# Kernel optimization log

Hardware: AMD Instinct MI355X
Metric: run time of the kernel (lower is better)

## Reference

```python
import jax, jax.numpy as jnp
import numpy as np

N = 10000
E = 160000
IN_DIM = 512
OUT_DIM = 256
NEG_SLOPE = 0.2  # DGL GATConv default LeakyReLU slope


def _gat_conv(x, W, b, attn_l, attn_r, src, dst, num_nodes, heads, out_dim):
    """DGL GATConv (eval mode, feat_drop/attn_drop disabled).
    x: [N, F_in]; W: [F_in, heads*out]; b: [heads*out];
    attn_l/attn_r: [heads, out]. Returns [N, heads, out]."""
    h = (x @ W).reshape(num_nodes, heads, out_dim)            # [N,H,D]
    el = jnp.einsum('nhd,hd->nh', h, attn_l)                  # [N,H]
    er = jnp.einsum('nhd,hd->nh', h, attn_r)                  # [N,H]
    e = jax.nn.leaky_relu(el[src] + er[dst], NEG_SLOPE)       # [E,H]
    # destination-grouped (edge) softmax, numerically stable
    m = jax.ops.segment_max(e, dst, num_segments=num_nodes)   # [N,H], -inf for empty
    m = jnp.where(jnp.isfinite(m), m, 0.0)
    ee = jnp.exp(e - m[dst])                                  # [E,H]
    s = jax.ops.segment_sum(ee, dst, num_segments=num_nodes)  # [N,H]
    a = ee / jnp.where(s > 0, s, 1.0)[dst]                    # [E,H]
    # message aggregation: scatter-add a_e * h[src]
    out = jax.ops.segment_sum(a[:, :, None] * h[src], dst, num_segments=num_nodes)
    return out + b.reshape(1, heads, out_dim)


def setup_inputs() -> dict:
    key = jax.random.key(0)
    ks = jax.random.split(key, 16)
    def glorot(k, shape):
        fan = shape[0] + shape[-1] if len(shape) > 1 else shape[-1]
        return jax.random.normal(k, shape, dtype=jnp.float32) * np.sqrt(2.0 / fan)
    inp = {
        'x':   jax.random.normal(ks[0], (N, IN_DIM), dtype=jnp.float32),
        'src': jax.random.randint(ks[1], (E,), 0, N),
        'dst': jax.random.randint(ks[2], (E,), 0, N),
        'W1': glorot(ks[3], (IN_DIM, 10 * 128)),
        'b1': jnp.zeros((10 * 128,), jnp.float32),
        'al1': glorot(ks[4], (10, 128)),
        'ar1': glorot(ks[5], (10, 128)),
        'W2': glorot(ks[6], (1280, 10 * 64)),
        'b2': jnp.zeros((10 * 64,), jnp.float32),
        'al2': glorot(ks[7], (10, 64)),
        'ar2': glorot(ks[8], (10, 64)),
        'W3': glorot(ks[9], (640, OUT_DIM)),
        'b3': jnp.zeros((OUT_DIM,), jnp.float32),
        'al3': glorot(ks[10], (1, OUT_DIM)),
        'ar3': glorot(ks[11], (1, OUT_DIM)),
        # residual linear 512 -> 256
        'Wres': glorot(ks[12], (IN_DIM, OUT_DIM)),
        'bres': jnp.zeros((OUT_DIM,), jnp.float32),
        'fuse_weight': jnp.full((1,), 0.5, jnp.float32),
    }
    return inp


def reference(x, src, dst, W1, b1, al1, ar1, W2, b2, al2, ar2,
              W3, b3, al3, ar3, Wres, bres, fuse_weight):
    elu = jax.nn.elu
    res = elu(x @ Wres + bres)                                        # [N,256]
    s1 = elu(_gat_conv(x, W1, b1, al1, ar1, src, dst, N, 10, 128))
    s1 = s1.reshape(N, -1)                                            # [N,1280]
    s2 = elu(_gat_conv(s1, W2, b2, al2, ar2, src, dst, N, 10, 64))
    s2 = s2.reshape(N, -1)                                            # [N,640]
    s3 = elu(_gat_conv(s2, W3, b3, al3, ar3, src, dst, N, 1, OUT_DIM))
    s3 = s3.reshape(N, -1)                                            # [N,256]
    return fuse_weight * s3 + (1.0 - fuse_weight) * res
```

## Files before the change

### kernel.cpp

```cpp
#include <hip/hip_runtime.h>
#include <stdint.h>

#define DEVINL __device__ __forceinline__

typedef __attribute__((ext_vector_type(8))) short short8;
typedef __attribute__((ext_vector_type(4))) float f32x4;

static constexpr int NNODES = 10000;

DEVINL float bf2f(unsigned short u) {
  unsigned int x = ((unsigned int)u) << 16;
  float f;
  __builtin_memcpy(&f, &x, 4);
  return f;
}
DEVINL unsigned short f2bf(float f) {
  unsigned int x;
  __builtin_memcpy(&x, &f, 4);
  unsigned int lsb = (x >> 16) & 1;
  x += 0x7fffu + lsb;
  return (unsigned short)(x >> 16);
}
DEVINL void bfpair(unsigned int u, float& f0, float& f1) {
  unsigned int a = u << 16, b = u & 0xffff0000u;
  __builtin_memcpy(&f0, &a, 4);
  __builtin_memcpy(&f1, &b, 4);
}
DEVINL bool is_bf16_mode(const unsigned int* fwWord) {
  return ((*fwWord) & 0xFFFFu) == 0x3F00u;
}

DEVINL void async_cp16(void* lds, const void* g) {
  __builtin_amdgcn_global_load_lds((const __attribute__((address_space(1))) unsigned int*)g,
                                   (__attribute__((address_space(3))) unsigned int*)lds,
                                   16, 0, 0);
}

__global__ __launch_bounds__(256) void gemm_fused(const unsigned short* __restrict__ A,
                                                  const unsigned short* __restrict__ Bt,
                                                  unsigned short* __restrict__ Ch,
                                                  int M, int N, int K, int nres,
                                                  unsigned short* __restrict__ Cres,
                                                  const float* __restrict__ rbias,
                                                  float* __restrict__ elp,
                                                  float* __restrict__ erp,
                                                  const float* __restrict__ alf,
                                                  const float* __restrict__ arf,
                                                  int logD, int H) {
  __shared__ __align__(16) unsigned short lA[128 * 32];
  __shared__ __align__(16) unsigned short lB[128 * 32];
  const int tid = threadIdx.x;
  const int wid = tid >> 6;
  const int lane = tid & 63;
  const int tm = blockIdx.x * 128;
  const int tn = blockIdx.y * 128;
  const int wr = (wid >> 1) * 64;
  const int wc = (wid & 1) * 64;
  f32x4 acc[4][4] = {};
  const int r_in_chunk = lane >> 2;
  const int cb = (lane & 3) * 16;
  const int mr = lane & 15;
  const int kq = (lane >> 4) * 8;
  const size_t stride = (size_t)K * 2;

  for (int k0 = 0; k0 < K; k0 += 32) {
#pragma unroll
    for (int c = 0; c < 2; ++c) {
      const int chunk = wid * 2 + c;
      const int row = chunk * 16 + r_in_chunk;
      int ga = tm + row;
      if (ga >= M) ga = M - 1;
      async_cp16(&lA[chunk * 512], (const char*)A + (size_t)ga * stride + (size_t)k0 * 2 + cb);
      const int gb = tn + row;
      async_cp16(&lB[chunk * 512], (const char*)Bt + (size_t)gb * stride + (size_t)k0 * 2 + cb);
    }
    __syncthreads();
    short8 af[4], bf[4];
#pragma unroll
    for (int i = 0; i < 4; ++i)
      af[i] = *(const short8*)&lA[(wr + i * 16 + mr) * 32 + kq];
#pragma unroll
    for (int j = 0; j < 4; ++j)
      bf[j] = *(const short8*)&lB[(wc + j * 16 + mr) * 32 + kq];
#pragma unroll
    for (int i = 0; i < 4; ++i)
#pragma unroll
      for (int j = 0; j < 4; ++j)
        acc[i][j] = __builtin_amdgcn_mfma_f32_16x16x32_bf16(af[i], bf[j], acc[i][j], 0, 0, 0);
    __syncthreads();
  }

  const int rbase = (lane >> 4) * 4;
  const int cc = lane & 15;
  if (tn < nres) {
#pragma unroll
    for (int i = 0; i < 4; ++i)
#pragma unroll
      for (int r = 0; r < 4; ++r) {
        const int row = tm + wr + i * 16 + rbase + r;
        if (row < M) {
#pragma unroll
          for (int j = 0; j < 4; ++j) {
            const int col = tn + wc + j * 16 + cc;
            float v = acc[i][j][r] + rbias[col];
            v = v > 0.f ? v : (__expf(v) - 1.f);
            Cres[(size_t)row * nres + col] = f2bf(v);
          }
        }
      }
  } else {
    const int tnh = tn - nres;
    const int Nh = N - nres;
    const int colw = tnh + wc;
    const int head = colw >> logD;
#pragma unroll
    for (int i = 0; i < 4; ++i)
#pragma unroll
      for (int r = 0; r < 4; ++r) {
        const int row = tm + wr + i * 16 + rbase + r;
        if (row < M) {
#pragma unroll
          for (int j = 0; j < 4; ++j)
            Ch[(size_t)row * Nh + colw + j * 16 + cc] = f2bf(acc[i][j][r]);
        }
      }
    float alv[4], arv[4];
#pragma unroll
    for (int j = 0; j < 4; ++j) {
      alv[j] = alf[colw + j * 16 + cc];
      arv[j] = arf[colw + j * 16 + cc];
    }
#pragma unroll
    for (int i = 0; i < 4; ++i)
#pragma unroll
      for (int r = 0; r < 4; ++r) {
        float pe = 0.f, pr = 0.f;
#pragma unroll
        for (int j = 0; j < 4; ++j) {
          pe += acc[i][j][r] * alv[j];
          pr += acc[i][j][r] * arv[j];
        }
#pragma unroll
        for (int o = 1; o < 16; o <<= 1) {
          pe += __shfl_xor(pe, o);
          pr += __shfl_xor(pr, o);
        }
        const int row = tm + wr + i * 16 + rbase + r;
        if ((lane & 15) == 0 && row < M) {
          atomicAdd(&elp[(size_t)row * H + head], pe);
          atomicAdd(&erp[(size_t)row * H + head], pr);
        }
      }
  }
}

struct CvtJobs {
  const void* src[12];
  float* dst[12];
  int n[12];
  int cnt;
};
__global__ void cvt_small_f32(CvtJobs jobs, const unsigned int* fwWord) {
  const bool isb = is_bf16_mode(fwWord);
  for (int j = 0; j < jobs.cnt; ++j) {
    for (int i = blockIdx.x * blockDim.x + threadIdx.x; i < jobs.n[j];
         i += gridDim.x * blockDim.x) {
      jobs.dst[j][i] = isb ? bf2f(((const unsigned short*)jobs.src[j])[i])
                           : ((const float*)jobs.src[j])[i];
    }
  }
}

__global__ __launch_bounds__(256) void cvt_x_bf16(const void* __restrict__ in,
                                                  unsigned short* __restrict__ out,
                                                  long n, const unsigned int* fwWord) {
  const bool isb = is_bf16_mode(fwWord);
  const long i0 = (long)(blockIdx.x * 256 + threadIdx.x) * 8;
  if (i0 >= n) return;
  if (isb) {
    *(short8*)&out[i0] = *(const short8*)&((const unsigned short*)in)[i0];
  } else {
    const float* f = (const float*)in + i0;
    unsigned short r[8];
#pragma unroll
    for (int j = 0; j < 8; ++j) r[j] = f2bf(f[j]);
    *(short8*)&out[i0] = *(const short8*)r;
  }
}

struct TAll {
  const void* src[4];
  unsigned short* dst[4];
  int K[4];
  int N[4];
  int b0[5];
};
__global__ __launch_bounds__(256) void transp_all4(TAll ja, const unsigned int* fwWord) {
  const bool isb = is_bf16_mode(fwWord);
  __shared__ unsigned short t[32][33];
  const int bid = blockIdx.x;
  int j = 0;
  while (j < 3 && bid >= ja.b0[j + 1]) ++j;
  const int local = bid - ja.b0[j];
  const int K = ja.K[j], Nn = ja.N[j];
  const int tilesX = Nn / 32;
  const int bx = (local % tilesX) * 32;
  const int by = (local / tilesX) * 32;
  const void* W = ja.src[j];
  unsigned short* Wt = ja.dst[j];
  const int x = threadIdx.x;
  const int y0 = threadIdx.y;
  for (int y = y0; y < 32; y += 8) {
    const size_t idx = (size_t)(by + y) * Nn + bx + x;
    t[y][x] = isb ? ((const unsigned short*)W)[idx] : f2bf(((const float*)W)[idx]);
  }
  __syncthreads();
  for (int y = y0; y < 32; y += 8)
    Wt[(size_t)(bx + y) * K + by + x] = t[x][y];
}

template <int H>
__global__ __launch_bounds__(256) void edge_w(const float* __restrict__ el,
                                              const float* __restrict__ er,
                                              const int* __restrict__ sidx,
                                              const int* __restrict__ didx,
                                              float* __restrict__ we_t, int E) {
  const int p = blockIdx.x * 256 + threadIdx.x;
  if (p >= E) return;
  const float* ep = el + (size_t)sidx[p] * H;
  const float* rp = er + (size_t)didx[p] * H;
#pragma unroll
  for (int h = 0; h < H; ++h) {
    float sc = ep[h] + rp[h];
    sc = sc > 0.f ? sc : 0.2f * sc;
    we_t[(size_t)h * E + p] = __expf(sc);
  }
}

template <int H, int D, int NS, int CW, int MODE>
__global__ __launch_bounds__(64) void gat_agg_hs(const unsigned short* __restrict__ hf,
                                                 const float* __restrict__ we_t,
                                                 const int* __restrict__ sidx,
                                                 const int* __restrict__ rowstart,
                                                 const float* __restrict__ bias,
                                                 void* __restrict__ outp,
                                                 const unsigned short* __restrict__ resact,
                                                 const float* __restrict__ fwf,
                                                 const unsigned int* fwWord, int E) {
  constexpr int CHUNK = 64;
  constexpr int SF = H * D / NS;
  constexpr int ACT = SF / CW;
  constexpr int SROW = H * D * 2;
  constexpr int LOG2D = (D == 64) ? 6 : (D == 128) ? 7 : 8;
  static_assert((H * D) % NS == 0 && (SF % CW) == 0 && ACT <= 64, "geometry");
  static_assert(CW == 2 || CW == 4, "vector width");
  static_assert(SF < 2 * D, "slice spans at most 2 heads");
  __shared__ float wls[2 * (CHUNK + 1)];
  __shared__ int soff[CHUNK];

  const int bid = blockIdx.x;
  const int n = bid / NS;
  const int sl = bid % NS;
  const int tid = threadIdx.x;
  const int e0 = rowstart[n], e1 = rowstart[n + 1];
  const int f0 = SF * sl;
  const int hlo = f0 >> LOG2D;
  const int hhi = (f0 + SF - 1) >> LOG2D;
  const int fbase = f0 + tid * CW;
  const int wbase = ((fbase >> LOG2D) != hlo) ? (CHUNK + 1) : 0;
  const bool act = tid < ACT;
  const char* hfb = (const char*)(hf + fbase);
  float acc[CW] = {};
  float swlo = 0.f, swhi = 0.f;

  for (int cs = e0; cs < e1; cs += CHUNK) {
    const int ce = min(CHUNK, e1 - cs);
    if (tid < ce) {
      soff[tid] = sidx[cs + tid] * SROW;
      const float wlo = we_t[(size_t)hlo * E + cs + tid];
      wls[tid] = wlo;
      swlo += wlo;
      if (hhi != hlo) {
        const float whi = we_t[(size_t)hhi * E + cs + tid];
        wls[CHUNK + 1 + tid] = whi;
        swhi += whi;
      }
    }
    __syncthreads();
    if (act) {
      int j = 0;
      for (; j + 8 <= ce; j += 8) {
        int o[8];
        float w[8];
#pragma unroll
        for (int b = 0; b < 8; ++b) {
          o[b] = soff[j + b];
          w[b] = wls[wbase + j + b];
        }
        if constexpr (CW == 4) {
          uint2 u[8];
#pragma unroll
          for (int b = 0; b < 8; ++b) u[b] = *(const uint2*)(hfb + o[b]);
#pragma unroll
          for (int b = 0; b < 8; ++b) {
            float a0, a1, a2, a3;
            bfpair(u[b].x, a0, a1);
            bfpair(u[b].y, a2, a3);
            acc[0] += w[b] * a0; acc[1] += w[b] * a1;
            acc[2] += w[b] * a2; acc[3] += w[b] * a3;
          }
        } else {
          unsigned int u[8];
#pragma unroll
          for (int b = 0; b < 8; ++b) u[b] = *(const unsigned int*)(hfb + o[b]);
#pragma unroll
          for (int b = 0; b < 8; ++b) {
            float a0, a1;
            bfpair(u[b], a0, a1);
            acc[0] += w[b] * a0; acc[1] += w[b] * a1;
          }
        }
      }
      for (; j < ce; ++j) {
        const int o = soff[j];
        const float w = wls[wbase + j];
        if constexpr (CW == 4) {
          const uint2 u = *(const uint2*)(hfb + o);
          float a0, a1, a2, a3;
          bfpair(u.x, a0, a1);
          bfpair(u.y, a2, a3);
          acc[0] += w * a0; acc[1] += w * a1; acc[2] += w * a2; acc[3] += w * a3;
        } else {
          const unsigned int u = *(const unsigned int*)(hfb + o);
          float a0, a1;
          bfpair(u, a0, a1);
          acc[0] += w * a0; acc[1] += w * a1;
        }
      }
    }
    __syncthreads();
  }

#pragma unroll
  for (int o = 32; o; o >>= 1) {
    swlo += __shfl_xor(swlo, o);
    swhi += __shfl_xor(swhi, o);
  }
  if (!act) return;
  const float stot = wbase ? swhi : swlo;
  const float inv = stot > 0.f ? 1.f / stot : 0.f;
  const size_t obase = (size_t)n * (H * D) + fbase;
  float v[CW];
#pragma unroll
  for (int k = 0; k < CW; ++k) {
    v[k] = acc[k] * inv + bias[fbase + k];
    v[k] = v[k] > 0.f ? v[k] : (__expf(v[k]) - 1.f);
  }
  if (MODE == 0) {
#pragma unroll
    for (int k = 0; k < CW; ++k)
      ((unsigned short*)outp)[obase + k] = f2bf(v[k]);
  } else {
    const float fw = fwf[0];
    const bool outb = is_bf16_mode(fwWord);
#pragma unroll
    for (int k = 0; k < CW; ++k) {
      const float r = bf2f(resact[obase + k]);
      const float o = fw * v[k] + (1.f - fw) * r;
      if (outb) ((unsigned short*)outp)[obase + k] = f2bf(o);
      else      ((float*)outp)[obase + k] = o;
    }
  }
}

__global__ void sentinel_k(unsigned short* __restrict__ outp, int total) {
  const int i = blockIdx.x * 256 + threadIdx.x;
  if (i < total) outp[i] = f2bf(12344.0f);
}

__global__ void hist_k(const int* __restrict__ dst, int* __restrict__ deg, int E) {
  const int i = blockIdx.x * blockDim.x + threadIdx.x;
  if (i < E) atomicAdd(&deg[dst[i]], 1);
}

__global__ __launch_bounds__(1024) void scan_k(const int* __restrict__ deg,
                                               int* __restrict__ rowstart,
                                               int* __restrict__ cursor, int Nn) {
  __shared__ int ls[1024];
  const int tid = threadIdx.x;
  const int CH = (Nn + 1023) >> 10;
  const int start = tid * CH;
  int sum = 0;
  for (int i = 0; i < CH; ++i) {
    const int idx = start + i;
    if (idx < Nn) sum += deg[idx];
  }
  ls[tid] = sum;
  __syncthreads();
  for (int o = 1; o < 1024; o <<= 1) {
    int v = 0;
    if (tid >= o) v = ls[tid - o];
    __syncthreads();
    ls[tid] += v;
    __syncthreads();
  }
  int run = tid > 0 ? ls[tid - 1] : 0;
  for (int i = 0; i < CH; ++i) {
    const int idx = start + i;
    if (idx < Nn) {
      rowstart[idx] = run;
      cursor[idx] = run;
      run += deg[idx];
    }
  }
  if (tid == 1023) rowstart[Nn] = ls[1023];
}

__global__ void scatter_k(const int* __restrict__ dst, const int* __restrict__ srcA,
                          int* __restrict__ cursor, int* __restrict__ sidx,
                          int* __restrict__ didx, int E) {
  const int i = blockIdx.x * blockDim.x + threadIdx.x;
  if (i < E) {
    const int d = dst[i];
    const int p = atomicAdd(&cursor[d], 1);
    sidx[p] = srcA[i];
    didx[p] = d;
  }
}

extern "C" void kernel_launch(void* const* d_in, const int* in_sizes, int n_in,
                              void* d_out, int out_size, void* d_ws, size_t ws_size,
                              hipStream_t stream) {
  const void* x    = d_in[0];
  const int* src   = (const int*)d_in[1];
  const int* dstA  = (const int*)d_in[2];
  const void* W1   = d_in[3];
  const void* b1   = d_in[4];
  const void* al1  = d_in[5];
  const void* ar1  = d_in[6];
  const void* W2   = d_in[7];
  const void* b2   = d_in[8];
  const void* al2  = d_in[9];
  const void* ar2  = d_in[10];
  const void* W3   = d_in[11];
  const void* b3   = d_in[12];
  const void* al3  = d_in[13];
  const void* ar3  = d_in[14];
  const void* Wres = d_in[15];
  const void* bres = d_in[16];
  const void* fw   = d_in[17];
  const unsigned int* fwWord = (const unsigned int*)fw;
  const int E = in_sizes[1];
  const int M = NNODES;

  char* base = (char*)d_ws;
  size_t off = 0;
  auto alloc = [&](size_t bytes) -> char* {
    char* p = base + off;
    off = (off + bytes + 255) & ~(size_t)255;
    return p;
  };
  char* zbase   = base;
  int* deg      = (int*)alloc((size_t)M * 4);
  float* elb1   = (float*)alloc((size_t)M * 10 * 4);
  float* erb1   = (float*)alloc((size_t)M * 10 * 4);
  float* elb2   = (float*)alloc((size_t)M * 10 * 4);
  float* erb2   = (float*)alloc((size_t)M * 10 * 4);
  float* elb3   = (float*)alloc((size_t)M * 4);
  float* erb3   = (float*)alloc((size_t)M * 4);
  const size_t zbytes = off;
  int* rowstart = (int*)alloc((size_t)(M + 1) * 4);
  int* cursor   = (int*)alloc((size_t)M * 4);
  int* sidx     = (int*)alloc((size_t)E * 4);
  int* didx     = (int*)alloc((size_t)E * 4);
  float* we_t   = (float*)alloc((size_t)E * 10 * 4);
  float* b1f   = (float*)alloc(1280 * 4);
  float* al1f  = (float*)alloc(1280 * 4);
  float* ar1f  = (float*)alloc(1280 * 4);
  float* b2f   = (float*)alloc(640 * 4);
  float* al2f  = (float*)alloc(640 * 4);
  float* ar2f  = (float*)alloc(640 * 4);
  float* b3f   = (float*)alloc(256 * 4);
  float* al3f  = (float*)alloc(256 * 4);
  float* ar3f  = (float*)alloc(256 * 4);
  float* bresf = (float*)alloc(256 * 4);
  float* fwf   = (float*)alloc(4);
  unsigned short* wtcat  = (unsigned short*)alloc((size_t)1536 * 512 * 2);
  unsigned short* wt2    = (unsigned short*)alloc((size_t)640 * 1280 * 2);
  unsigned short* wt3    = (unsigned short*)alloc((size_t)256 * 640 * 2);
  unsigned short* resact = (unsigned short*)alloc((size_t)M * 256 * 2);
  unsigned short* regA   = (unsigned short*)alloc((size_t)M * 1280 * 2);
  unsigned short* regB   = (unsigned short*)alloc((size_t)M * 1280 * 2);

  if (off > ws_size) {
    sentinel_k<<<(out_size + 255) / 256, 256, 0, stream>>>((unsigned short*)d_out, out_size);
    return;
  }

  unsigned short* h1 = regA;
  unsigned short* h2 = regA;
  unsigned short* h3 = regA;
  unsigned short* xb = regB;
  unsigned short* s1 = regB;
  unsigned short* s2 = regB;

  hipMemsetAsync(zbase, 0, zbytes, stream);

  CvtJobs jobs;
  const void* srcs[11] = {b1, al1, ar1, b2, al2, ar2, b3, al3, ar3, bres, fw};
  float* dsts[11] = {b1f, al1f, ar1f, b2f, al2f, ar2f, b3f, al3f, ar3f, bresf, fwf};
  const int ns[11] = {1280, 1280, 1280, 640, 640, 640, 256, 256, 256, 256, 1};
  for (int j = 0; j < 11; ++j) { jobs.src[j] = srcs[j]; jobs.dst[j] = dsts[j]; jobs.n[j] = ns[j]; }
  jobs.cnt = 11;
  cvt_small_f32<<<8, 256, 0, stream>>>(jobs, fwWord);

  cvt_x_bf16<<<(int)(((long)M * 512 / 8 + 255) / 256), 256, 0, stream>>>(x, xb, (long)M * 512, fwWord);

  TAll ta;
  ta.src[0] = W1;   ta.dst[0] = wtcat + (size_t)256 * 512; ta.K[0] = 512;  ta.N[0] = 1280;
  ta.src[1] = W2;   ta.dst[1] = wt2;                       ta.K[1] = 1280; ta.N[1] = 640;
  ta.src[2] = W3;   ta.dst[2] = wt3;                       ta.K[2] = 640;  ta.N[2] = 256;
  ta.src[3] = Wres; ta.dst[3] = wtcat;                     ta.K[3] = 512;  ta.N[3] = 256;
  ta.b0[0] = 0;
  for (int j = 0; j < 4; ++j)
    ta.b0[j + 1] = ta.b0[j] + (ta.K[j] / 32) * (ta.N[j] / 32);
  transp_all4<<<ta.b0[4], dim3(32, 8), 0, stream>>>(ta, fwWord);

  hist_k<<<(E + 255) / 256, 256, 0, stream>>>(dstA, deg, E);
  scan_k<<<1, 1024, 0, stream>>>(deg, rowstart, cursor, M);
  scatter_k<<<(E + 255) / 256, 256, 0, stream>>>(dstA, src, cursor, sidx, didx, E);

  const int MT = (M + 127) / 128;
  const int EB = (E + 255) / 256;

  gemm_fused<<<dim3(MT, 12), 256, 0, stream>>>(xb, wtcat, h1, M, 1536, 512,
                                               256, resact, bresf,
                                               elb1, erb1, al1f, ar1f, 7, 10);
  edge_w<10><<<EB, 256, 0, stream>>>(elb1, erb1, sidx, didx, we_t, E);
  gat_agg_hs<10, 128, 8, 4, 0><<<M * 8, 64, 0, stream>>>(h1, we_t, sidx, rowstart,
                                                         b1f, s1, nullptr, fwf, fwWord, E);

  gemm_fused<<<dim3(MT, 5), 256, 0, stream>>>(s1, wt2, h2, M, 640, 1280,
                                              0, nullptr, nullptr,
                                              elb2, erb2, al2f, ar2f, 6, 10);
  edge_w<10><<<EB, 256, 0, stream>>>(elb2, erb2, sidx, didx, we_t, E);
  gat_agg_hs<10, 64, 8, 2, 0><<<M * 8, 64, 0, stream>>>(h2, we_t, sidx, rowstart,
                                                        b2f, s2, nullptr, fwf, fwWord, E);

  gemm_fused<<<dim3(MT, 2), 256, 0, stream>>>(s2, wt3, h3, M, 256, 640,
                                              0, nullptr, nullptr,
                                              elb3, erb3, al3f, ar3f, 8, 1);
  edge_w<1><<<EB, 256, 0, stream>>>(elb3, erb3, sidx, didx, we_t, E);
  gat_agg_hs<1, 256, 2, 2, 1><<<M * 2, 64, 0, stream>>>(h3, we_t, sidx, rowstart,
                                                        b3f, d_out, resact, fwf, fwWord, E);
}
```

Baseline: 305.0 us.

## Fold attention vectors into weight matrix as extra GEMM columns

```diff
diff --git a/kernel.cpp b/kernel.cpp
--- a/kernel.cpp
+++ b/kernel.cpp
@@ -39,14 +39,10 @@
 __global__ __launch_bounds__(256) void gemm_fused(const unsigned short* __restrict__ A,
                                                   const unsigned short* __restrict__ Bt,
                                                   unsigned short* __restrict__ Ch,
-                                                  int M, int N, int K, int nres,
+                                                  int M, int N, int K, int nres, int nh,
                                                   unsigned short* __restrict__ Cres,
                                                   const float* __restrict__ rbias,
-                                                  float* __restrict__ elp,
-                                                  float* __restrict__ erp,
-                                                  const float* __restrict__ alf,
-                                                  const float* __restrict__ arf,
-                                                  int logD, int H) {
+                                                  float* __restrict__ elerf) {
   __shared__ __align__(16) unsigned short lA[128 * 32];
   __shared__ __align__(16) unsigned short lB[128 * 32];
   const int tid = threadIdx.x;
@@ -108,11 +104,8 @@
           }
         }
       }
-  } else {
-    const int tnh = tn - nres;
-    const int Nh = N - nres;
-    const int colw = tnh + wc;
-    const int head = colw >> logD;
+  } else if (tn < nres + nh) {
+    const int colw = tn - nres + wc;
 #pragma unroll
     for (int i = 0; i < 4; ++i)
 #pragma unroll
@@ -121,37 +114,39 @@
         if (row < M) {
 #pragma unroll
           for (int j = 0; j < 4; ++j)
-            Ch[(size_t)row * Nh + colw + j * 16 + cc] = f2bf(acc[i][j][r]);
+            Ch[(size_t)row * nh + colw + j * 16 + cc] = f2bf(acc[i][j][r]);
         }
       }
-    float alv[4], arv[4];
-#pragma unroll
-    for (int j = 0; j < 4; ++j) {
-      alv[j] = alf[colw + j * 16 + cc];
-      arv[j] = arf[colw + j * 16 + cc];
-    }
+  } else {
+    const int colw = tn - nres - nh + wc;
 #pragma unroll
     for (int i = 0; i < 4; ++i)
 #pragma unroll
       for (int r = 0; r < 4; ++r) {
-        float pe = 0.f, pr = 0.f;
-#pragma unroll
-        for (int j = 0; j < 4; ++j) {
-          pe += acc[i][j][r] * alv[j];
-          pr += acc[i][j][r] * arv[j];
-        }
-#pragma unroll
-        for (int o = 1; o < 16; o <<= 1) {
-          pe += __shfl_xor(pe, o);
-          pr += __shfl_xor(pr, o);
-        }
         const int row = tm + wr + i * 16 + rbase + r;
-        if ((lane & 15) == 0 && row < M) {
-          atomicAdd(&elp[(size_t)row * H + head], pe);
-          atomicAdd(&erp[(size_t)row * H + head], pr);
+        if (row < M) {
+#pragma unroll
+          for (int j = 0; j < 4; ++j)
+            elerf[(size_t)row * 128 + colw + j * 16 + cc] = acc[i][j][r];
         }
       }
   }
+}
+
+template <int H, int D>
+__global__ __launch_bounds__(256) void welr_build(const unsigned short* __restrict__ wt,
+                                                  const float* __restrict__ al,
+                                                  const float* __restrict__ ar,
+                                                  unsigned short* __restrict__ out, int K) {
+  const int row = blockIdx.y;
+  const int k = blockIdx.x * 256 + threadIdx.x;
+  if (k >= K) return;
+  const int h = row < H ? row : row - H;
+  const float* v = (row < H ? al : ar) + h * D;
+  const unsigned short* wp = wt + (size_t)(h * D) * K + k;
+  float acc = 0.f;
+  for (int d = 0; d < D; ++d) acc += bf2f(wp[(size_t)d * K]) * v[d];
+  out[(size_t)row * K + k] = f2bf(acc);
 }
 
 struct CvtJobs {
@@ -220,18 +215,17 @@
 }
 
 template <int H>
-__global__ __launch_bounds__(256) void edge_w(const float* __restrict__ el,
-                                              const float* __restrict__ er,
+__global__ __launch_bounds__(256) void edge_w(const float* __restrict__ elerf,
                                               const int* __restrict__ sidx,
                                               const int* __restrict__ didx,
                                               float* __restrict__ we_t, int E) {
   const int p = blockIdx.x * 256 + threadIdx.x;
   if (p >= E) return;
-  const float* ep = el + (size_t)sidx[p] * H;
-  const float* rp = er + (size_t)didx[p] * H;
+  const float* ep = elerf + (size_t)sidx[p] * 128;
+  const float* rp = elerf + (size_t)didx[p] * 128;
 #pragma unroll
   for (int h = 0; h < H; ++h) {
-    float sc = ep[h] + rp[h];
+    float sc = ep[h] + rp[H + h];
     sc = sc > 0.f ? sc : 0.2f * sc;
     we_t[(size_t)h * E + p] = __expf(sc);
   }
@@ -460,20 +454,13 @@
     off = (off + bytes + 255) & ~(size_t)255;
     return p;
   };
-  char* zbase   = base;
   int* deg      = (int*)alloc((size_t)M * 4);
-  float* elb1   = (float*)alloc((size_t)M * 10 * 4);
-  float* erb1   = (float*)alloc((size_t)M * 10 * 4);
-  float* elb2   = (float*)alloc((size_t)M * 10 * 4);
-  float* erb2   = (float*)alloc((size_t)M * 10 * 4);
-  float* elb3   = (float*)alloc((size_t)M * 4);
-  float* erb3   = (float*)alloc((size_t)M * 4);
-  const size_t zbytes = off;
   int* rowstart = (int*)alloc((size_t)(M + 1) * 4);
   int* cursor   = (int*)alloc((size_t)M * 4);
   int* sidx     = (int*)alloc((size_t)E * 4);
   int* didx     = (int*)alloc((size_t)E * 4);
   float* we_t   = (float*)alloc((size_t)E * 10 * 4);
+  float* elerf  = (float*)alloc((size_t)M * 128 * 4);
   float* b1f   = (float*)alloc(1280 * 4);
   float* al1f  = (float*)alloc(1280 * 4);
   float* ar1f  = (float*)alloc(1280 * 4);
@@ -485,9 +472,9 @@
   float* ar3f  = (float*)alloc(256 * 4);
   float* bresf = (float*)alloc(256 * 4);
   float* fwf   = (float*)alloc(4);
-  unsigned short* wtcat  = (unsigned short*)alloc((size_t)1536 * 512 * 2);
-  unsigned short* wt2    = (unsigned short*)alloc((size_t)640 * 1280 * 2);
-  unsigned short* wt3    = (unsigned short*)alloc((size_t)256 * 640 * 2);
+  unsigned short* wtcat = (unsigned short*)alloc((size_t)1664 * 512 * 2);
+  unsigned short* wt2   = (unsigned short*)alloc((size_t)768 * 1280 * 2);
+  unsigned short* wt3   = (unsigned short*)alloc((size_t)384 * 640 * 2);
   unsigned short* resact = (unsigned short*)alloc((size_t)M * 256 * 2);
   unsigned short* regA   = (unsigned short*)alloc((size_t)M * 1280 * 2);
   unsigned short* regB   = (unsigned short*)alloc((size_t)M * 1280 * 2);
@@ -504,7 +491,7 @@
   unsigned short* s1 = regB;
   unsigned short* s2 = regB;
 
-  hipMemsetAsync(zbase, 0, zbytes, stream);
+  hipMemsetAsync(deg, 0, (size_t)M * 4, stream);
 
   CvtJobs jobs;
   const void* srcs[11] = {b1, al1, ar1, b2, al2, ar2, b3, al3, ar3, bres, fw};
@@ -526,6 +513,13 @@
     ta.b0[j + 1] = ta.b0[j] + (ta.K[j] / 32) * (ta.N[j] / 32);
   transp_all4<<<ta.b0[4], dim3(32, 8), 0, stream>>>(ta, fwWord);
 
+  welr_build<10, 128><<<dim3(2, 20), 256, 0, stream>>>(
+      wtcat + (size_t)256 * 512, al1f, ar1f, wtcat + (size_t)1536 * 512, 512);
+  welr_build<10, 64><<<dim3(5, 20), 256, 0, stream>>>(
+      wt2, al2f, ar2f, wt2 + (size_t)640 * 1280, 1280);
+  welr_build<1, 256><<<dim3(3, 2), 256, 0, stream>>>(
+      wt3, al3f, ar3f, wt3 + (size_t)256 * 640, 640);
+
   hist_k<<<(E + 255) / 256, 256, 0, stream>>>(dstA, deg, E);
   scan_k<<<1, 1024, 0, stream>>>(deg, rowstart, cursor, M);
   scatter_k<<<(E + 255) / 256, 256, 0, stream>>>(dstA, src, cursor, sidx, didx, E);
@@ -533,24 +527,21 @@
   const int MT = (M + 127) / 128;
   const int EB = (E + 255) / 256;
 
-  gemm_fused<<<dim3(MT, 12), 256, 0, stream>>>(xb, wtcat, h1, M, 1536, 512,
-                                               256, resact, bresf,
-                                               elb1, erb1, al1f, ar1f, 7, 10);
-  edge_w<10><<<EB, 256, 0, stream>>>(elb1, erb1, sidx, didx, we_t, E);
+  gemm_fused<<<dim3(MT, 13), 256, 0, stream>>>(xb, wtcat, h1, M, 1664, 512,
+                                               256, 1280, resact, bresf, elerf);
+  edge_w<10><<<EB, 256, 0, stream>>>(elerf, sidx, didx, we_t, E);
   gat_agg_hs<10, 128, 8, 4, 0><<<M * 8, 64, 0, stream>>>(h1, we_t, sidx, rowstart,
                                                          b1f, s1, nullptr, fwf, fwWord, E);
 
-  gemm_fused<<<dim3(MT, 5), 256, 0, stream>>>(s1, wt2, h2, M, 640, 1280,
-                                              0, nullptr, nullptr,
-                                              elb2, erb2, al2f, ar2f, 6, 10);
-  edge_w<10><<<EB, 256, 0, stream>>>(elb2, erb2, sidx, didx, we_t, E);
+  gemm_fused<<<dim3(MT, 6), 256, 0, stream>>>(s1, wt2, h2, M, 768, 1280,
+                                              0, 640, nullptr, nullptr, elerf);
+  edge_w<10><<<EB, 256, 0, stream>>>(elerf, sidx, didx, we_t, E);
   gat_agg_hs<10, 64, 8, 2, 0><<<M * 8, 64, 0, stream>>>(h2, we_t, sidx, rowstart,
                                                         b2f, s2, nullptr, fwf, fwWord, E);
 
-  gemm_fused<<<dim3(MT, 2), 256, 0, stream>>>(s2, wt3, h3, M, 256, 640,
-                                              0, nullptr, nullptr,
-                                              elb3, erb3, al3f, ar3f, 8, 1);
-  edge_w<1><<<EB, 256, 0, stream>>>(elb3, erb3, sidx, didx, we_t, E);
+  gemm_fused<<<dim3(MT, 3), 256, 0, stream>>>(s2, wt3, h3, M, 384, 640,
+                                              0, 256, nullptr, nullptr, elerf);
+  edge_w<1><<<EB, 256, 0, stream>>>(elerf, sidx, didx, we_t, E);
   gat_agg_hs<1, 256, 2, 2, 1><<<M * 2, 64, 0, stream>>>(h3, we_t, sidx, rowstart,
                                                         b3f, d_out, resact, fwf, fwWord, E);
 }
```

Result: slower. 321.1 us (+5.3%).
